# Optimization experiments

Hardware: AMD Instinct MI355X
Metric: run time of the kernel (lower is better)

## Reference

```python
import jax, jax.numpy as jnp
import numpy as np


def _conv(x, w, b, stride, pad):
    # NCHW conv, OIHW weights, bias add
    y = jax.lax.conv_general_dilated(
        x, w, (stride, stride), [(pad, pad), (pad, pad)],
        dimension_numbers=('NCHW', 'OIHW', 'NCHW'))
    return y + b[None, :, None, None]


def setup_inputs() -> dict:
    key = jax.random.key(0)
    ks = jax.random.split(key, 8)
    s = 0.05  # small init so SiLU chains stay numerically tame
    f32 = jnp.float32
    return {
        'x': jax.random.normal(ks[0], (8, 3, 640, 640), f32),
        'w0': jax.random.normal(ks[1], (32, 3, 3, 3), f32) * s,
        'b0': jnp.zeros((32,), f32),
        'w1': jax.random.normal(ks[2], (64, 32, 3, 3), f32) * s,
        'b1': jnp.zeros((64,), f32),
        'wc0': jax.random.normal(ks[3], (64, 64, 1, 1), f32) * s,
        'bc0': jnp.zeros((64,), f32),
        'wb1': jax.random.normal(ks[4], (32, 32, 3, 3), f32) * s,
        'bb1': jnp.zeros((32,), f32),
        'wb2': jax.random.normal(ks[5], (32, 32, 3, 3), f32) * s,
        'bb2': jnp.zeros((32,), f32),
        'wc1': jax.random.normal(ks[6], (64, 96, 1, 1), f32) * s,
        'bc1': jnp.zeros((64,), f32),
        'w3': jax.random.normal(ks[7], (128, 64, 3, 3), f32) * s,
        'b3': jnp.zeros((128,), f32),
    }


def reference(x, w0, b0, w1, b1, wc0, bc0, wb1, bb1, wb2, bb2, wc1, bc1, w3, b3):
    silu = jax.nn.silu
    # stem: conv0 (s2) + conv1 (s2), each Conv+SiLU
    h = silu(_conv(x, w0, b0, 2, 1))     # [B,32,320,320]
    h = silu(_conv(h, w1, b1, 2, 1))     # [B,64,160,160]
    # C2f block: 1x1 conv, split channels in half, residual bottleneck, concat, 1x1 conv
    y = silu(_conv(h, wc0, bc0, 1, 0))   # [B,64,160,160]
    x1, x2 = jnp.split(y, 2, axis=1)     # each [B,32,160,160]
    b = silu(_conv(x2, wb1, bb1, 1, 1))
    b = silu(_conv(b, wb2, bb2, 1, 1))
    b = x2 + b                           # shortcut=True bottleneck
    cat = jnp.concatenate([x1, x2, b], axis=1)  # [B,96,160,160] == 192*w
    h = silu(_conv(cat, wc1, bc1, 1, 0))  # [B,64,160,160]
    # conv3: downsample stage (s2)
    out = silu(_conv(h, w3, b3, 2, 1))    # [B,128,80,80]
    return out
```

## Files before the change

### kernel.cpp

```cpp
#include <hip/hip_runtime.h>
#include <hip/hip_bf16.h>

typedef __attribute__((ext_vector_type(8))) short short8;
typedef __attribute__((ext_vector_type(16))) float f32x16;
typedef __attribute__((ext_vector_type(4))) float f32x4;
typedef __attribute__((ext_vector_type(4))) unsigned int uint4v;
typedef __attribute__((ext_vector_type(4))) unsigned short ushort4v;

__device__ __forceinline__ float silu_f(float v) {
    return v * __builtin_amdgcn_rcpf(1.0f + __expf(-v));
}
__device__ __forceinline__ unsigned short bfhi(float v) {
    __hip_bfloat16 h = __float2bfloat16(v);
    return *reinterpret_cast<unsigned short*>(&h);
}
__device__ __forceinline__ float bf2f(unsigned short u) {
    __hip_bfloat16 h;
    *reinterpret_cast<unsigned short*>(&h) = u;
    return __bfloat162float(h);
}

__global__ __launch_bounds__(256) void prep_small(
    const float* __restrict__ w1, const float* __restrict__ wc0,
    const float* __restrict__ wb1, const float* __restrict__ wb2,
    const float* __restrict__ wc1, const float* __restrict__ w0,
    unsigned short* __restrict__ arena)
{
    const int u = blockIdx.x * 256 + threadIdx.x;
    if (u >= 6016) return;
    const int lane = u & 63, pf = u >> 6;
    float wv[8];
    if (pf < 36) {
        const int q = pf, cc = q & 1, rnd = (q >> 1) & 1, tap = q >> 2;
        const int co = cc * 32 + (lane & 31), ci0 = rnd * 16 + (lane >> 5) * 8;
        #pragma unroll
        for (int j = 0; j < 8; ++j) wv[j] = w1[(co * 32 + ci0 + j) * 9 + tap];
    } else if (pf < 44) {
        const int q = pf - 36, cc = q & 1, rnd = q >> 1;
        const int co = cc * 32 + (lane & 31), ci0 = rnd * 16 + (lane >> 5) * 8;
        #pragma unroll
        for (int j = 0; j < 8; ++j) wv[j] = wc0[co * 64 + ci0 + j];
    } else if (pf < 62) {
        const int q = pf - 44, rnd = q & 1, tap = q >> 1;
        const int co = lane & 31, ci0 = rnd * 16 + (lane >> 5) * 8;
        #pragma unroll
        for (int j = 0; j < 8; ++j) wv[j] = wb1[(co * 32 + ci0 + j) * 9 + tap];
    } else if (pf < 80) {
        const int q = pf - 62, rnd = q & 1, tap = q >> 1;
        const int co = lane & 31, ci0 = rnd * 16 + (lane >> 5) * 8;
        #pragma unroll
        for (int j = 0; j < 8; ++j) wv[j] = wb2[(co * 32 + ci0 + j) * 9 + tap];
    } else if (pf < 92) {
        const int q = pf - 80, cc = q & 1, rnd = q >> 1;
        const int co = cc * 32 + (lane & 31), ci0 = rnd * 16 + (lane >> 5) * 8;
        #pragma unroll
        for (int j = 0; j < 8; ++j) wv[j] = wc1[co * 96 + ci0 + j];
    } else {
        const int co = lane & 31;
        const int k0 = (pf - 92) * 16 + (lane >> 5) * 8;
        #pragma unroll
        for (int j = 0; j < 8; ++j) {
            const int k = k0 + j;
            wv[j] = (k < 27) ? w0[(co * 3 + k / 9) * 9 + (k % 9)] : 0.0f;
        }
    }
    unsigned short hs[8], ls[8];
    #pragma unroll
    for (int j = 0; j < 8; ++j) {
        unsigned short hh = bfhi(wv[j]);
        hs[j] = hh; ls[j] = bfhi(wv[j] - bf2f(hh));
    }
    *reinterpret_cast<short8*>(&arena[pf * 1024 + lane * 8])       = *(short8*)hs;
    *reinterpret_cast<short8*>(&arena[pf * 1024 + 512 + lane * 8]) = *(short8*)ls;
}

__global__ __launch_bounds__(256) void prep_w3(
    const float* __restrict__ w3, unsigned short* __restrict__ arena)
{
    const int u = blockIdx.x * 256 + threadIdx.x;
    const int lane = u & 63, pf = u >> 6;
    const int cc = pf & 1, rr = (pf >> 1) & 3, t9 = pf >> 3;
    const int tap = t9 % 9, cg = t9 / 9;
    const int co = cg * 64 + cc * 32 + (lane & 31);
    const int ci0 = rr * 16 + (lane >> 5) * 8;
    unsigned short hs[8], ls[8];
    #pragma unroll
    for (int j = 0; j < 8; ++j) {
        float wv = w3[(co * 64 + ci0 + j) * 9 + tap];
        unsigned short hh = bfhi(wv);
        hs[j] = hh; ls[j] = bfhi(wv - bf2f(hh));
    }
    *reinterpret_cast<short8*>(&arena[pf * 1024 + lane * 8])       = *(short8*)hs;
    *reinterpret_cast<short8*>(&arena[pf * 1024 + 512 + lane * 8]) = *(short8*)ls;
}

__global__ __launch_bounds__(512, 4) void conv0_mfma(
    const float* __restrict__ x, const unsigned short* __restrict__ wfr,
    const float* __restrict__ bias, unsigned short* __restrict__ out)
{
    const int tid = threadIdx.x;
    const int wv = tid >> 6, lane = tid & 63;
    const int p = lane & 31, h = lane >> 5;
    const int plane = blockIdx.y;
    const int pyp = plane >> 1, pxp = plane & 1;
    const int pp = blockIdx.x * 256 + wv * 32 + p;
    const int n = blockIdx.z;
    const int Y = 2 * (pp / 160) + pyp, X = 2 * (pp % 160) + pxp;

    int off[16]; float msk[16];
    #pragma unroll
    for (int rnd = 0; rnd < 2; ++rnd)
        #pragma unroll
        for (int j = 0; j < 8; ++j) {
            const int kidx = rnd * 16 + h * 8 + j;
            const int idx = rnd * 8 + j;
            if (kidx < 27) {
                const int ci = kidx / 9, tap = kidx - ci * 9;
                const int iy = 2 * Y + (tap / 3) - 1;
                const int ix = 2 * X + (tap % 3) - 1;
                const bool ok = (iy >= 0) && (iy < 640) && (ix >= 0) && (ix < 640);
                const int cy = min(max(iy, 0), 639), cx = min(max(ix, 0), 639);
                off[idx] = ci * 409600 + cy * 640 + cx;
                msk[idx] = ok ? 1.0f : 0.0f;
            } else {
                off[idx] = 0; msk[idx] = 0.0f;
            }
        }

    f32x16 acc;
    #pragma unroll
    for (int q = 0; q < 4; ++q) {
        f32x4 b4 = *reinterpret_cast<const f32x4*>(&bias[q * 8 + 4 * h]);
        #pragma unroll
        for (int r = 0; r < 4; ++r) acc[q * 4 + r] = b4[r];
    }

    const float* xb = x + (long)n * 1228800;
    #pragma unroll
    for (int rnd = 0; rnd < 2; ++rnd) {
        unsigned short hs[8], ls[8];
        #pragma unroll
        for (int j = 0; j < 8; ++j) {
            float v = xb[off[rnd * 8 + j]] * msk[rnd * 8 + j];
            unsigned short hh = bfhi(v);
            hs[j] = hh; ls[j] = bfhi(v - bf2f(hh));
        }
        short8 Bh = *(short8*)hs, Bl = *(short8*)ls;
        const unsigned short* fb = wfr + (92 + rnd) * 1024 + lane * 8;
        short8 Awh = *reinterpret_cast<const short8*>(fb);
        short8 Awl = *reinterpret_cast<const short8*>(fb + 512);
        acc = __builtin_amdgcn_mfma_f32_32x32x16_bf16(Awh, Bh, acc, 0, 0, 0);
        acc = __builtin_amdgcn_mfma_f32_32x32x16_bf16(Awh, Bl, acc, 0, 0, 0);
        acc = __builtin_amdgcn_mfma_f32_32x32x16_bf16(Awl, Bh, acc, 0, 0, 0);
    }

    unsigned short* op = out + (((long)n * 4 + plane) * 25600 + pp) * 64;
    #pragma unroll
    for (int q = 0; q < 4; ++q) {
        ushort4v hv, lv;
        #pragma unroll
        for (int r = 0; r < 4; ++r) {
            float v = silu_f(acc[q * 4 + r]);
            unsigned short hh = bfhi(v);
            hv[r] = hh; lv[r] = bfhi(v - bf2f(hh));
        }
        *reinterpret_cast<ushort4v*>(op + q * 16 + 4 * h)     = hv;
        *reinterpret_cast<ushort4v*>(op + q * 16 + 8 + 4 * h) = lv;
    }
}

__global__ __launch_bounds__(256, 4) void conv1_fused(
    const unsigned short* __restrict__ h0, const unsigned short* __restrict__ wfr,
    const unsigned short* __restrict__ wc0fr, const float* __restrict__ bias,
    const float* __restrict__ bc0, unsigned short* __restrict__ ycl)
{
    __shared__ unsigned short lds[10400];
    const int tid = threadIdx.x;
    const int wv = tid >> 6, lane = tid & 63;
    const int p = lane & 31, h = lane >> 5;
    const int r = wv >> 1, cc = wv & 1;
    const int bx = blockIdx.x % 5, by = blockIdx.x / 5;
    const int ox0 = bx * 32, oy0 = by * 2;
    const int n = blockIdx.z;

    f32x16 acc;
    #pragma unroll
    for (int q = 0; q < 4; ++q) {
        f32x4 b4 = *reinterpret_cast<const f32x4*>(&bias[cc * 32 + q * 8 + 4 * h]);
        #pragma unroll
        for (int r2 = 0; r2 < 4; ++r2) acc[q * 4 + r2] = b4[r2];
    }

    for (int c = 0; c < 2; ++c) {
        __syncthreads();
        for (int u = tid; u < 1300; u += 256) {
            const int rec = u >> 2, s = u & 3;
            int gp, row, col;
            if (rec < 64)       { gp = 0; row = rec >> 5;  col = rec & 31; }
            else if (rec < 130) { gp = 1; int r2 = rec - 64;  row = r2 / 33; col = r2 - row * 33; }
            else if (rec < 226) { gp = 2; int r2 = rec - 130; row = r2 >> 5; col = r2 & 31; }
            else                { gp = 3; int r2 = rec - 226; row = r2 / 33; col = r2 - row * 33; }
            const int gr = (gp >= 2) ? oy0 - 1 + row : oy0 + row;
            const int gc = (gp & 1)  ? ox0 - 1 + col : ox0 + col;
            uint4v val = {0, 0, 0, 0};
            if (gr >= 0 && gr < 160 && gc >= 0 && gc < 160)
                val = *reinterpret_cast<const uint4v*>(
                    h0 + (((long)n * 4 + gp) * 25600 + gr * 160 + gc) * 64 + (4 * c + s) * 8);
            *reinterpret_cast<uint4v*>(&lds[rec * 32 + ((s ^ ((rec >> 1) & 3)) * 8)]) = val;
        }
        __syncthreads();

        #pragma unroll
        for (int tap = 0; tap < 9; ++tap) {
            const int dy = tap / 3 - 1, dx = tap % 3 - 1;
            const int ppy = dy & 1, ppx = dx & 1;
            const int toy = ppy ? ((dy == -1) ? 0 : 1) : 0;
            const int tox = ppx ? ((dx == -1) ? 0 : 1) : 0;
            const int gp = ppy * 2 + ppx;
            const int base = (gp == 0) ? 0 : (gp == 1) ? 64 : (gp == 2) ? 130 : 226;
            const int W = ppx ? 33 : 32;
            const int rec = base + (ppy ? (r + toy) : r) * W + (p + tox);
            const unsigned short* t = &lds[rec * 32];
            const int pm = (rec >> 1) & 3;
            short8 Bh = *reinterpret_cast<const short8*>(t + (((2 * h)     ^ pm) * 8));
            short8 Bl = *reinterpret_cast<const short8*>(t + (((2 * h + 1) ^ pm) * 8));
            const unsigned short* fb = wfr + ((tap * 2 + c) * 2 + cc) * 1024 + lane * 8;
            short8 Awh = *reinterpret_cast<const short8*>(fb);
            short8 Awl = *reinterpret_cast<const short8*>(fb + 512);
            acc = __builtin_amdgcn_mfma_f32_32x32x16_bf16(Awh, Bh, acc, 0, 0, 0);
            acc = __builtin_amdgcn_mfma_f32_32x32x16_bf16(Awh, Bl, acc, 0, 0, 0);
            acc = __builtin_amdgcn_mfma_f32_32x32x16_bf16(Awl, Bh, acc, 0, 0, 0);
        }
    }

    __syncthreads();
    {
        const int rec2 = r * 32 + p;
        #pragma unroll
        for (int q = 0; q < 4; ++q) {
            ushort4v hv, lv;
            #pragma unroll
            for (int r2 = 0; r2 < 4; ++r2) {
                float v = silu_f(acc[q * 4 + r2]);
                unsigned short hh = bfhi(v);
                hv[r2] = hh; lv[r2] = bfhi(v - bf2f(hh));
            }
            const int lsh = (2 * (cc * 4 + q))     ^ (rec2 & 15);
            const int lsl = (2 * (cc * 4 + q) + 1) ^ (rec2 & 15);
            *reinterpret_cast<ushort4v*>(&lds[rec2 * 128 + lsh * 8 + 4 * h]) = hv;
            *reinterpret_cast<ushort4v*>(&lds[rec2 * 128 + lsl * 8 + 4 * h]) = lv;
        }
    }
    __syncthreads();

    f32x16 a2;
    #pragma unroll
    for (int q = 0; q < 4; ++q) {
        f32x4 b4 = *reinterpret_cast<const f32x4*>(&bc0[cc * 32 + q * 8 + 4 * h]);
        #pragma unroll
        for (int r2 = 0; r2 < 4; ++r2) a2[q * 4 + r2] = b4[r2];
    }
    {
        const int rec2 = r * 32 + p;
        #pragma unroll
        for (int rnd = 0; rnd < 4; ++rnd) {
            const int sh = (4 * rnd + 2 * h)     ^ (rec2 & 15);
            const int sl = (4 * rnd + 2 * h + 1) ^ (rec2 & 15);
            short8 Bh = *reinterpret_cast<const short8*>(&lds[rec2 * 128 + sh * 8]);
            short8 Bl = *reinterpret_cast<const short8*>(&lds[rec2 * 128 + sl * 8]);
            const unsigned short* fb = wc0fr + (rnd * 2 + cc) * 1024 + lane * 8;
            short8 Awh = *reinterpret_cast<const short8*>(fb);
            short8 Awl = *reinterpret_cast<const short8*>(fb + 512);
            a2 = __builtin_amdgcn_mfma_f32_32x32x16_bf16(Awh, Bh, a2, 0, 0, 0);
            a2 = __builtin_amdgcn_mfma_f32_32x32x16_bf16(Awh, Bl, a2, 0, 0, 0);
            a2 = __builtin_amdgcn_mfma_f32_32x32x16_bf16(Awl, Bh, a2, 0, 0, 0);
        }
    }

    const int oy = oy0 + r;
    unsigned short* op = ycl + ((long)n * 25600 + (long)oy * 160 + ox0 + p) * 128;
    #pragma unroll
    for (int q = 0; q < 4; ++q) {
        ushort4v hv, lv;
        #pragma unroll
        for (int r2 = 0; r2 < 4; ++r2) {
            float v = silu_f(a2[q * 4 + r2]);
            unsigned short hh = bfhi(v);
            hv[r2] = hh; lv[r2] = bfhi(v - bf2f(hh));
        }
        const int gq = cc * 4 + q;
        *reinterpret_cast<ushort4v*>(op + gq * 16 + 4 * h)     = hv;
        *reinterpret_cast<ushort4v*>(op + gq * 16 + 8 + 4 * h) = lv;
    }
}

template <bool RESID>
__global__ __launch_bounds__(512, 4) void wb3x3(
    const unsigned short* __restrict__ in, int inRec, int inSlot0,
    const unsigned short* __restrict__ wfr, const float* __restrict__ bias,
    unsigned short* __restrict__ outb, const unsigned short* __restrict__ resid)
{
    __shared__ unsigned short lds[21760];
    const int tid = threadIdx.x;
    const int wv = tid >> 6, lane = tid & 63;
    const int p = lane & 31, h = lane >> 5;
    const int bx = blockIdx.x % 5, by = blockIdx.x / 5;
    const int ox0 = bx * 32, oy0 = by * 8;
    const int n = blockIdx.z;

    for (int u = tid; u < 2720; u += 512) {
        const int rec = u >> 3, s = u & 7;
        const int row = rec / 34, col = rec - row * 34;
        const int gr = oy0 - 1 + row, gc = ox0 - 1 + col;
        uint4v val = {0, 0, 0, 0};
        if (gr >= 0 && gr < 160 && gc >= 0 && gc < 160)
            val = *reinterpret_cast<const uint4v*>(
                in + ((long)n * 25600 + gr * 160 + gc) * inRec + (inSlot0 + s) * 8);
        *reinterpret_cast<uint4v*>(&lds[rec * 64 + ((s ^ (rec & 7)) * 8)]) = val;
    }

    f32x16 acc;
    #pragma unroll
    for (int q = 0; q < 4; ++q) {
        f32x4 b4 = *reinterpret_cast<const f32x4*>(&bias[q * 8 + 4 * h]);
        #pragma unroll
        for (int r = 0; r < 4; ++r) acc[q * 4 + r] = b4[r];
    }
    __syncthreads();

    #pragma unroll
    for (int tap = 0; tap < 9; ++tap) {
        const int dy = tap / 3 - 1, dx = tap % 3 - 1;
        const int rec = (wv + dy + 1) * 34 + (p + dx + 1);
        const unsigned short* t = &lds[rec * 64];
        short8 Bh[2], Bl[2];
        #pragma unroll
        for (int rnd = 0; rnd < 2; ++rnd) {
            Bh[rnd] = *reinterpret_cast<const short8*>(t + (((rnd*4 + 2*h)     ^ (rec & 7)) * 8));
            Bl[rnd] = *reinterpret_cast<const short8*>(t + (((rnd*4 + 2*h + 1) ^ (rec & 7)) * 8));
        }
        #pragma unroll
        for (int rnd = 0; rnd < 2; ++rnd) {
            const unsigned short* fb = wfr + (tap * 2 + rnd) * 1024 + lane * 8;
            short8 Awh = *reinterpret_cast<const short8*>(fb);
            short8 Awl = *reinterpret_cast<const short8*>(fb + 512);
            acc = __builtin_amdgcn_mfma_f32_32x32x16_bf16(Awh, Bh[rnd], acc, 0, 0, 0);
            acc = __builtin_amdgcn_mfma_f32_32x32x16_bf16(Awh, Bl[rnd], acc, 0, 0, 0);
            acc = __builtin_amdgcn_mfma_f32_32x32x16_bf16(Awl, Bh[rnd], acc, 0, 0, 0);
        }
    }

    const int oy = oy0 + wv;
    const long prow = (long)n * 25600 + (long)oy * 160 + ox0 + p;
    unsigned short* op = outb + prow * 64;
    const unsigned short* rp = RESID ? resid + prow * 128 : nullptr;
    #pragma unroll
    for (int q = 0; q < 4; ++q) {
        ushort4v hv, lv;
        float vs[4];
        #pragma unroll
        for (int r = 0; r < 4; ++r) vs[r] = silu_f(acc[q * 4 + r]);
        if (RESID) {
            ushort4v rh = *reinterpret_cast<const ushort4v*>(rp + (q + 4) * 16 + 4 * h);
            ushort4v rl = *reinterpret_cast<const ushort4v*>(rp + (q + 4) * 16 + 8 + 4 * h);
            #pragma unroll
            for (int r = 0; r < 4; ++r) vs[r] += bf2f(rh[r]) + bf2f(rl[r]);
        }
        #pragma unroll
        for (int r = 0; r < 4; ++r) {
            unsigned short hh = bfhi(vs[r]);
            hv[r] = hh; lv[r] = bfhi(vs[r] - bf2f(hh));
        }
        *reinterpret_cast<ushort4v*>(op + q * 16 + 4 * h)     = hv;
        *reinterpret_cast<ushort4v*>(op + q * 16 + 8 + 4 * h) = lv;
    }
}

template <int R1, int R2, bool POUT>
__global__ __launch_bounds__(512, 4) void wc1x1(
    const unsigned short* __restrict__ in1, int rec1,
    const unsigned short* __restrict__ in2, int rec2,
    const unsigned short* __restrict__ wfr, const float* __restrict__ bias,
    unsigned short* __restrict__ outb)
{
    constexpr int RT = R1 + R2;
    const int tid = threadIdx.x;
    const int wv = tid >> 6, lane = tid & 63;
    const int p = lane & 31, h = lane >> 5;
    const int n = blockIdx.z;
    const int px0 = blockIdx.x * 512;

    f32x16 acc[2][2];
    #pragma unroll
    for (int cc = 0; cc < 2; ++cc)
        #pragma unroll
        for (int q = 0; q < 4; ++q) {
            f32x4 b4 = *reinterpret_cast<const f32x4*>(&bias[cc * 32 + q * 8 + 4 * h]);
            #pragma unroll
            for (int r = 0; r < 4; ++r) { acc[cc][0][q*4+r] = b4[r]; acc[cc][1][q*4+r] = b4[r]; }
        }

    #pragma unroll
    for (int rnd = 0; rnd < RT; ++rnd) {
        const unsigned short* bp = (rnd < R1) ? in1 : in2;
        const int recN = (rnd < R1) ? rec1 : rec2;
        const int s0 = 4 * ((rnd < R1) ? rnd : rnd - R1);
        #pragma unroll
        for (int k = 0; k < 2; ++k) {
            const int px = px0 + (wv * 2 + k) * 32 + p;
            const unsigned short* sp = bp + ((long)n * 25600 + px) * recN + (s0 + 2 * h) * 8;
            short8 Bh = *reinterpret_cast<const short8*>(sp);
            short8 Bl = *reinterpret_cast<const short8*>(sp + 8);
            #pragma unroll
            for (int cc = 0; cc < 2; ++cc) {
                const unsigned short* fb = wfr + (rnd * 2 + cc) * 1024 + lane * 8;
                short8 Awh = *reinterpret_cast<const short8*>(fb);
                short8 Awl = *reinterpret_cast<const short8*>(fb + 512);
                acc[cc][k] = __builtin_amdgcn_mfma_f32_32x32x16_bf16(Awh, Bh, acc[cc][k], 0, 0, 0);
                acc[cc][k] = __builtin_amdgcn_mfma_f32_32x32x16_bf16(Awh, Bl, acc[cc][k], 0, 0, 0);
                acc[cc][k] = __builtin_amdgcn_mfma_f32_32x32x16_bf16(Awl, Bh, acc[cc][k], 0, 0, 0);
            }
        }
    }

    #pragma unroll
    for (int k = 0; k < 2; ++k) {
        const int px = px0 + (wv * 2 + k) * 32 + p;
        unsigned short* op;
        if (POUT) {
            const int y = px / 160, xx = px % 160;
            const int pl = (y & 1) * 2 + (xx & 1);
            op = outb + (((long)n * 4 + pl) * 6400 + (y >> 1) * 80 + (xx >> 1)) * 128;
        } else {
            op = outb + ((long)n * 25600 + px) * 128;
        }
        #pragma unroll
        for (int cc = 0; cc < 2; ++cc)
            #pragma unroll
            for (int q = 0; q < 4; ++q) {
                ushort4v hv, lv;
                #pragma unroll
                for (int r = 0; r < 4; ++r) {
                    float v = silu_f(acc[cc][k][q * 4 + r]);
                    unsigned short hh = bfhi(v);
                    hv[r] = hh; lv[r] = bfhi(v - bf2f(hh));
                }
                const int gq = cc * 4 + q;
                *reinterpret_cast<ushort4v*>(op + gq * 16 + 4 * h)     = hv;
                *reinterpret_cast<ushort4v*>(op + gq * 16 + 8 + 4 * h) = lv;
            }
    }
}

__global__ __launch_bounds__(512, 4) void conv3_one(
    const unsigned short* __restrict__ h2p, const unsigned short* __restrict__ wfr,
    const float* __restrict__ bias, float* __restrict__ outf)
{
    __shared__ unsigned short lds[34848];
    const int tid = threadIdx.x;
    const int wv = tid >> 6, lane = tid & 63;
    const int p = lane & 31, h = lane >> 5;
    const int bx = blockIdx.x % 5, by = blockIdx.x / 5;
    const int ox0 = bx * 16, oy0 = by * 16;
    const int cg = blockIdx.y;
    const int co0 = cg * 64;
    const int n = blockIdx.z;

    f32x16 acc[2];
    #pragma unroll
    for (int cc = 0; cc < 2; ++cc)
        #pragma unroll
        for (int q = 0; q < 4; ++q) {
            f32x4 b4 = *reinterpret_cast<const f32x4*>(&bias[co0 + cc * 32 + q * 8 + 4 * h]);
            #pragma unroll
            for (int r = 0; r < 4; ++r) acc[cc][q * 4 + r] = b4[r];
        }

    for (int rr = 0; rr < 4; ++rr) {
        __syncthreads();
        for (int u = tid; u < 4356; u += 512) {
            const int rec = u >> 2, s = u & 3;
            int gp, row, col;
            if (rec < 256)      { gp = 0; row = rec >> 4; col = rec & 15; }
            else if (rec < 528) { gp = 1; int r2 = rec - 256; row = r2 / 17; col = r2 - row * 17; }
            else if (rec < 800) { gp = 2; int r2 = rec - 528; row = r2 >> 4; col = r2 & 15; }
            else                { gp = 3; int r2 = rec - 800; row = r2 / 17; col = r2 - row * 17; }
            const int gr = (gp >= 2) ? oy0 - 1 + row : oy0 + row;
            const int gc = (gp & 1)  ? ox0 - 1 + col : ox0 + col;
            uint4v val = {0, 0, 0, 0};
            if (gr >= 0 && gr < 80 && gc >= 0 && gc < 80)
                val = *reinterpret_cast<const uint4v*>(
                    h2p + (((long)n * 4 + gp) * 6400 + gr * 80 + gc) * 128 + (rr * 4 + s) * 8);
            *reinterpret_cast<uint4v*>(&lds[rec * 32 + ((s ^ ((rec >> 1) & 3)) * 8)]) = val;
        }
        __syncthreads();

        #pragma unroll
        for (int tap = 0; tap < 9; ++tap) {
            const int dy = tap / 3 - 1, dx = tap % 3 - 1;
            const int ppy = dy & 1, ppx = dx & 1;
            const int toy = ppy ? ((dy == -1) ? 0 : 1) : 0;
            const int tox = ppx ? ((dx == -1) ? 0 : 1) : 0;
            const int gp = ppy * 2 + ppx;
            const int base = (gp == 0) ? 0 : (gp == 1) ? 256 : (gp == 2) ? 528 : 800;
            const int W = ppx ? 17 : 16;
            const int rl = wv * 2 + (p >> 4), cl = p & 15;
            const int rec = base + (ppy ? (rl + toy) : rl) * W + (cl + tox);
            const unsigned short* t = &lds[rec * 32];
            const int pm = (rec >> 1) & 3;
            short8 Bh = *reinterpret_cast<const short8*>(t + (((2*h)     ^ pm) * 8));
            short8 Bl = *reinterpret_cast<const short8*>(t + (((2*h + 1) ^ pm) * 8));
            #pragma unroll
            for (int cc = 0; cc < 2; ++cc) {
                const unsigned short* fb =
                    wfr + (((cg * 9 + tap) * 4 + rr) * 2 + cc) * 1024 + lane * 8;
                short8 Awh = *reinterpret_cast<const short8*>(fb);
                short8 Awl = *reinterpret_cast<const short8*>(fb + 512);
                acc[cc] = __builtin_amdgcn_mfma_f32_32x32x16_bf16(Awh, Bh, acc[cc], 0, 0, 0);
                acc[cc] = __builtin_amdgcn_mfma_f32_32x32x16_bf16(Awh, Bl, acc[cc], 0, 0, 0);
                acc[cc] = __builtin_amdgcn_mfma_f32_32x32x16_bf16(Awl, Bh, acc[cc], 0, 0, 0);
            }
        }
    }

    const int rl = wv * 2 + (p >> 4);
    const int oy = oy0 + rl;
    const int pxg = oy * 80 + ox0 + (p & 15);
    #pragma unroll
    for (int cc = 0; cc < 2; ++cc)
        #pragma unroll
        for (int q = 0; q < 4; ++q)
            #pragma unroll
            for (int r = 0; r < 4; ++r) {
                const int co = co0 + cc * 32 + q * 8 + 4 * h + r;
                outf[((long)n * 128 + co) * 6400 + pxg] = silu_f(acc[cc][q * 4 + r]);
            }
}

extern "C" void kernel_launch(void* const* d_in, const int* in_sizes, int n_in,
                              void* d_out, int out_size, void* d_ws, size_t ws_size,
                              hipStream_t stream) {
    const float* x   = (const float*)d_in[0];
    const float* w0  = (const float*)d_in[1];
    const float* b0  = (const float*)d_in[2];
    const float* w1  = (const float*)d_in[3];
    const float* b1  = (const float*)d_in[4];
    const float* wc0 = (const float*)d_in[5];
    const float* bc0 = (const float*)d_in[6];
    const float* wb1 = (const float*)d_in[7];
    const float* bb1 = (const float*)d_in[8];
    const float* wb2 = (const float*)d_in[9];
    const float* bb2 = (const float*)d_in[10];
    const float* wc1 = (const float*)d_in[11];
    const float* bc1 = (const float*)d_in[12];
    const float* w3  = (const float*)d_in[13];
    const float* b3  = (const float*)d_in[14];

    unsigned short* u = (unsigned short*)d_ws;
    unsigned short* h0p  = u;
    unsigned short* ycl  = u + 52428800L;
    unsigned short* b1cl = u + 26214400L;
    unsigned short* bcl  = u + 39321600L;
    unsigned short* h2p  = u;
    unsigned short* w3a  = u + 26214400L;

    unsigned short* wsa = (unsigned short*)d_out;
    unsigned short* a_conv1 = wsa;
    unsigned short* a_wc0   = wsa + 36 * 1024;
    unsigned short* a_wb1   = wsa + 44 * 1024;
    unsigned short* a_wb2   = wsa + 62 * 1024;
    unsigned short* a_wc1   = wsa + 80 * 1024;

    prep_small<<<dim3(24, 1, 1), dim3(256, 1, 1), 0, stream>>>(
        w1, wc0, wb1, wb2, wc1, w0, wsa);

    conv0_mfma<<<dim3(100, 4, 8), dim3(512, 1, 1), 0, stream>>>(x, wsa, b0, h0p);

    conv1_fused<<<dim3(400, 1, 8), dim3(256, 1, 1), 0, stream>>>(
        h0p, a_conv1, a_wc0, b1, bc0, ycl);

    wb3x3<false><<<dim3(100, 1, 8), dim3(512, 1, 1), 0, stream>>>(
        ycl, 128, 8, a_wb1, bb1, b1cl, nullptr);

    wb3x3<true><<<dim3(100, 1, 8), dim3(512, 1, 1), 0, stream>>>(
        b1cl, 64, 0, a_wb2, bb2, bcl, ycl);

    prep_w3<<<dim3(36, 1, 1), dim3(256, 1, 1), 0, stream>>>(w3, w3a);

    wc1x1<4, 2, true><<<dim3(50, 1, 8), dim3(512, 1, 1), 0, stream>>>(
        ycl, 128, bcl, 64, a_wc1, bc1, h2p);

    conv3_one<<<dim3(25, 2, 8), dim3(512, 1, 1), 0, stream>>>(h2p, w3a, b3, (float*)d_out);
}
```

Measured before the change: 275.4 us.

## Fuse conv0 into conv1 kernel, recomputing stem tile halo in LDS

Merges the stride-2 conv0 kernel into the conv1 kernel. Each block computes the conv0 outputs its conv1 tile needs, halo included, directly from the fp32 input and writes them as split bf16 hi/lo into a doubled LDS buffer. This removes the global write and re-read of the large h0 intermediate and one kernel launch. In exchange, halo rows and columns are recomputed by neighbouring blocks, LDS use doubles to about 41KB (which may lower occupancy), and it adds a warp-uniform fast path for interior tiles that skips bounds checks.

```diff
diff --git a/kernel.cpp b/kernel.cpp
--- a/kernel.cpp
+++ b/kernel.cpp
@@ -94,87 +94,13 @@
     *reinterpret_cast<short8*>(&arena[pf * 1024 + 512 + lane * 8]) = *(short8*)ls;
 }
 
-__global__ __launch_bounds__(512, 4) void conv0_mfma(
+__global__ __launch_bounds__(256, 4) void stem_fused(
     const float* __restrict__ x, const unsigned short* __restrict__ wfr,
-    const float* __restrict__ bias, unsigned short* __restrict__ out)
+    const unsigned short* __restrict__ wc0fr, const float* __restrict__ b0,
+    const float* __restrict__ bias, const float* __restrict__ bc0,
+    unsigned short* __restrict__ ycl)
 {
-    const int tid = threadIdx.x;
-    const int wv = tid >> 6, lane = tid & 63;
-    const int p = lane & 31, h = lane >> 5;
-    const int plane = blockIdx.y;
-    const int pyp = plane >> 1, pxp = plane & 1;
-    const int pp = blockIdx.x * 256 + wv * 32 + p;
-    const int n = blockIdx.z;
-    const int Y = 2 * (pp / 160) + pyp, X = 2 * (pp % 160) + pxp;
-
-    int off[16]; float msk[16];
-    #pragma unroll
-    for (int rnd = 0; rnd < 2; ++rnd)
-        #pragma unroll
-        for (int j = 0; j < 8; ++j) {
-            const int kidx = rnd * 16 + h * 8 + j;
-            const int idx = rnd * 8 + j;
-            if (kidx < 27) {
-                const int ci = kidx / 9, tap = kidx - ci * 9;
-                const int iy = 2 * Y + (tap / 3) - 1;
-                const int ix = 2 * X + (tap % 3) - 1;
-                const bool ok = (iy >= 0) && (iy < 640) && (ix >= 0) && (ix < 640);
-                const int cy = min(max(iy, 0), 639), cx = min(max(ix, 0), 639);
-                off[idx] = ci * 409600 + cy * 640 + cx;
-                msk[idx] = ok ? 1.0f : 0.0f;
-            } else {
-                off[idx] = 0; msk[idx] = 0.0f;
-            }
-        }
-
-    f32x16 acc;
-    #pragma unroll
-    for (int q = 0; q < 4; ++q) {
-        f32x4 b4 = *reinterpret_cast<const f32x4*>(&bias[q * 8 + 4 * h]);
-        #pragma unroll
-        for (int r = 0; r < 4; ++r) acc[q * 4 + r] = b4[r];
-    }
-
-    const float* xb = x + (long)n * 1228800;
-    #pragma unroll
-    for (int rnd = 0; rnd < 2; ++rnd) {
-        unsigned short hs[8], ls[8];
-        #pragma unroll
-        for (int j = 0; j < 8; ++j) {
-            float v = xb[off[rnd * 8 + j]] * msk[rnd * 8 + j];
-            unsigned short hh = bfhi(v);
-            hs[j] = hh; ls[j] = bfhi(v - bf2f(hh));
-        }
-        short8 Bh = *(short8*)hs, Bl = *(short8*)ls;
-        const unsigned short* fb = wfr + (92 + rnd) * 1024 + lane * 8;
-        short8 Awh = *reinterpret_cast<const short8*>(fb);
-        short8 Awl = *reinterpret_cast<const short8*>(fb + 512);
-        acc = __builtin_amdgcn_mfma_f32_32x32x16_bf16(Awh, Bh, acc, 0, 0, 0);
-        acc = __builtin_amdgcn_mfma_f32_32x32x16_bf16(Awh, Bl, acc, 0, 0, 0);
-        acc = __builtin_amdgcn_mfma_f32_32x32x16_bf16(Awl, Bh, acc, 0, 0, 0);
-    }
-
-    unsigned short* op = out + (((long)n * 4 + plane) * 25600 + pp) * 64;
-    #pragma unroll
-    for (int q = 0; q < 4; ++q) {
-        ushort4v hv, lv;
-        #pragma unroll
-        for (int r = 0; r < 4; ++r) {
-            float v = silu_f(acc[q * 4 + r]);
-            unsigned short hh = bfhi(v);
-            hv[r] = hh; lv[r] = bfhi(v - bf2f(hh));
-        }
-        *reinterpret_cast<ushort4v*>(op + q * 16 + 4 * h)     = hv;
-        *reinterpret_cast<ushort4v*>(op + q * 16 + 8 + 4 * h) = lv;
-    }
-}
-
-__global__ __launch_bounds__(256, 4) void conv1_fused(
-    const unsigned short* __restrict__ h0, const unsigned short* __restrict__ wfr,
-    const unsigned short* __restrict__ wc0fr, const float* __restrict__ bias,
-    const float* __restrict__ bc0, unsigned short* __restrict__ ycl)
-{
-    __shared__ unsigned short lds[10400];
+    __shared__ unsigned short lds[20800];
     const int tid = threadIdx.x;
     const int wv = tid >> 6, lane = tid & 63;
     const int p = lane & 31, h = lane >> 5;
@@ -182,6 +108,105 @@
     const int bx = blockIdx.x % 5, by = blockIdx.x / 5;
     const int ox0 = bx * 32, oy0 = by * 2;
     const int n = blockIdx.z;
+    const float* xb = x + (long)n * 1228800;
+
+    const int h8 = h * 8;
+    int doff[16];
+    #pragma unroll
+    for (int idx = 0; idx < 16; ++idx) {
+        const int k = (idx >> 3) * 16 + h8 + (idx & 7);
+        if (k < 27) {
+            const int ci = (k * 57) >> 9;
+            const int tap = k - 9 * ci;
+            const int dy = (tap * 11) >> 5, dx = tap - 3 * dy;
+            doff[idx] = ci * 409600 + (dy - 1) * 640 + (dx - 1);
+        } else {
+            doff[idx] = 0;
+        }
+    }
+
+    for (int it = 0; it < 3; ++it) {
+        const int g = it * 4 + wv;
+        if (g < 11) {
+            const int rc = g * 32 + p;
+            const bool validR = rc < 325;
+            const int rec_c = validR ? rc : 324;
+            int gp, row, col;
+            if (rec_c < 64)       { gp = 0; row = rec_c >> 5; col = rec_c & 31; }
+            else if (rec_c < 130) { gp = 1; int r2 = rec_c - 64;  row = r2 / 33; col = r2 - row * 33; }
+            else if (rec_c < 226) { gp = 2; int r2 = rec_c - 130; row = r2 >> 5; col = r2 & 31; }
+            else                  { gp = 3; int r2 = rec_c - 226; row = r2 / 33; col = r2 - row * 33; }
+            const int gr = (gp >= 2) ? oy0 - 1 + row : oy0 + row;
+            const int gc = (gp & 1)  ? ox0 - 1 + col : ox0 + col;
+            const bool valid = validR && ((unsigned)gr < 160u) && ((unsigned)gc < 160u);
+            const int Y = 2 * gr + (gp >> 1);
+            const int X = 2 * gc + (gp & 1);
+            const int Bsafe = valid ? (1280 * Y + 2 * X) : 641;
+            const bool interior = valid && gr > 0 && gr < 159 && gc > 0 && gc < 159;
+            const bool fastw = __all(interior);
+
+            f32x16 a0;
+            #pragma unroll
+            for (int q = 0; q < 4; ++q) {
+                f32x4 b4 = *reinterpret_cast<const f32x4*>(&b0[q * 8 + 4 * h]);
+                #pragma unroll
+                for (int r2 = 0; r2 < 4; ++r2) a0[q * 4 + r2] = b4[r2];
+            }
+
+            #pragma unroll
+            for (int rnd = 0; rnd < 2; ++rnd) {
+                unsigned short hs[8], ls[8];
+                if (fastw) {
+                    #pragma unroll
+                    for (int j = 0; j < 8; ++j) {
+                        float v = xb[Bsafe + doff[rnd * 8 + j]];
+                        if (rnd == 1 && j >= 3) v = (h == 0) ? v : 0.0f;
+                        unsigned short hh = bfhi(v);
+                        hs[j] = hh; ls[j] = bfhi(v - bf2f(hh));
+                    }
+                } else {
+                    #pragma unroll
+                    for (int j = 0; j < 8; ++j) {
+                        const int k = rnd * 16 + h8 + j;
+                        const int ci = (k * 57) >> 9;
+                        const int tap = k - 9 * ci;
+                        const int dy = (tap * 11) >> 5, dx = tap - 3 * dy;
+                        const int iy = 2 * Y + dy - 1;
+                        const int ix = 2 * X + dx - 1;
+                        bool ok = valid && ((unsigned)iy < 640u) && ((unsigned)ix < 640u);
+                        if (rnd == 1 && j >= 3) ok = ok && (h == 0);
+                        float v = ok ? xb[Bsafe + doff[rnd * 8 + j]] : 0.0f;
+                        unsigned short hh = bfhi(v);
+                        hs[j] = hh; ls[j] = bfhi(v - bf2f(hh));
+                    }
+                }
+                short8 Bh = *(short8*)hs, Bl = *(short8*)ls;
+                const unsigned short* fb = wfr + (92 + rnd) * 1024 + lane * 8;
+                short8 Awh = *reinterpret_cast<const short8*>(fb);
+                short8 Awl = *reinterpret_cast<const short8*>(fb + 512);
+                a0 = __builtin_amdgcn_mfma_f32_32x32x16_bf16(Awh, Bh, a0, 0, 0, 0);
+                a0 = __builtin_amdgcn_mfma_f32_32x32x16_bf16(Awh, Bl, a0, 0, 0, 0);
+                a0 = __builtin_amdgcn_mfma_f32_32x32x16_bf16(Awl, Bh, a0, 0, 0, 0);
+            }
+
+            if (validR) {
+                const int pm = rc & 7;
+                #pragma unroll
+                for (int q = 0; q < 4; ++q) {
+                    ushort4v hv, lv;
+                    #pragma unroll
+                    for (int r2 = 0; r2 < 4; ++r2) {
+                        float v = valid ? silu_f(a0[q * 4 + r2]) : 0.0f;
+                        unsigned short hh = bfhi(v);
+                        hv[r2] = hh; lv[r2] = bfhi(v - bf2f(hh));
+                    }
+                    *reinterpret_cast<ushort4v*>(&lds[rc * 64 + (((2 * q)     ^ pm) * 8) + 4 * h]) = hv;
+                    *reinterpret_cast<ushort4v*>(&lds[rc * 64 + (((2 * q + 1) ^ pm) * 8) + 4 * h]) = lv;
+                }
+            }
+        }
+    }
+    __syncthreads();
 
     f32x16 acc;
     #pragma unroll
@@ -190,26 +215,8 @@
         #pragma unroll
         for (int r2 = 0; r2 < 4; ++r2) acc[q * 4 + r2] = b4[r2];
     }
-
+    #pragma unroll
     for (int c = 0; c < 2; ++c) {
-        __syncthreads();
-        for (int u = tid; u < 1300; u += 256) {
-            const int rec = u >> 2, s = u & 3;
-            int gp, row, col;
-            if (rec < 64)       { gp = 0; row = rec >> 5;  col = rec & 31; }
-            else if (rec < 130) { gp = 1; int r2 = rec - 64;  row = r2 / 33; col = r2 - row * 33; }
-            else if (rec < 226) { gp = 2; int r2 = rec - 130; row = r2 >> 5; col = r2 & 31; }
-            else                { gp = 3; int r2 = rec - 226; row = r2 / 33; col = r2 - row * 33; }
-            const int gr = (gp >= 2) ? oy0 - 1 + row : oy0 + row;
-            const int gc = (gp & 1)  ? ox0 - 1 + col : ox0 + col;
-            uint4v val = {0, 0, 0, 0};
-            if (gr >= 0 && gr < 160 && gc >= 0 && gc < 160)
-                val = *reinterpret_cast<const uint4v*>(
-                    h0 + (((long)n * 4 + gp) * 25600 + gr * 160 + gc) * 64 + (4 * c + s) * 8);
-            *reinterpret_cast<uint4v*>(&lds[rec * 32 + ((s ^ ((rec >> 1) & 3)) * 8)]) = val;
-        }
-        __syncthreads();
-
         #pragma unroll
         for (int tap = 0; tap < 9; ++tap) {
             const int dy = tap / 3 - 1, dx = tap % 3 - 1;
@@ -220,10 +227,10 @@
             const int base = (gp == 0) ? 0 : (gp == 1) ? 64 : (gp == 2) ? 130 : 226;
             const int W = ppx ? 33 : 32;
             const int rec = base + (ppy ? (r + toy) : r) * W + (p + tox);
-            const unsigned short* t = &lds[rec * 32];
-            const int pm = (rec >> 1) & 3;
-            short8 Bh = *reinterpret_cast<const short8*>(t + (((2 * h)     ^ pm) * 8));
-            short8 Bl = *reinterpret_cast<const short8*>(t + (((2 * h + 1) ^ pm) * 8));
+            const unsigned short* t = &lds[rec * 64];
+            const int pm = rec & 7;
+            short8 Bh = *reinterpret_cast<const short8*>(t + (((4 * c + 2 * h)     ^ pm) * 8));
+            short8 Bl = *reinterpret_cast<const short8*>(t + (((4 * c + 2 * h + 1) ^ pm) * 8));
             const unsigned short* fb = wfr + ((tap * 2 + c) * 2 + cc) * 1024 + lane * 8;
             short8 Awh = *reinterpret_cast<const short8*>(fb);
             short8 Awl = *reinterpret_cast<const short8*>(fb + 512);
@@ -557,7 +564,6 @@
     const float* b3  = (const float*)d_in[14];
 
     unsigned short* u = (unsigned short*)d_ws;
-    unsigned short* h0p  = u;
     unsigned short* ycl  = u + 52428800L;
     unsigned short* b1cl = u + 26214400L;
     unsigned short* bcl  = u + 39321600L;
@@ -574,10 +580,8 @@
     prep_small<<<dim3(24, 1, 1), dim3(256, 1, 1), 0, stream>>>(
         w1, wc0, wb1, wb2, wc1, w0, wsa);
 
-    conv0_mfma<<<dim3(100, 4, 8), dim3(512, 1, 1), 0, stream>>>(x, wsa, b0, h0p);
-
-    conv1_fused<<<dim3(400, 1, 8), dim3(256, 1, 1), 0, stream>>>(
-        h0p, a_conv1, a_wc0, b1, bc0, ycl);
+    stem_fused<<<dim3(400, 1, 8), dim3(256, 1, 1), 0, stream>>>(
+        x, a_conv1, a_wc0, b0, b1, bc0, ycl);
 
     wb3x3<false><<<dim3(100, 1, 8), dim3(512, 1, 1), 0, stream>>>(
         ycl, 128, 8, a_wb1, bb1, b1cl, nullptr);
```

Measured after the change: 246.2 us. -10.6%, faster.
